# Kernel tuning notes

Hardware: AMD Instinct MI355X
Metric: run time of the kernel (lower is better)

## Reference

```python
import jax, jax.numpy as jnp
import numpy as np

TOPK = 9
NUM_CLASSES = 80
EPS = 1e-9
IMG = 1280
STRIDES = (8, 16, 32)


def _make_anchors():
    boxes = []
    for s in STRIDES:
        n = IMG // s
        c = (np.arange(n, dtype=np.float32) + 0.5) * s
        cy, cx = np.meshgrid(c, c, indexing='ij')
        cx = cx.reshape(-1); cy = cy.reshape(-1)
        half = s * 2.5
        boxes.append(np.stack([cx - half, cy - half, cx + half, cy + half], axis=-1))
    return jnp.asarray(np.concatenate(boxes, axis=0), jnp.float32)


def setup_inputs() -> dict:
    key = jax.random.key(0)
    k1, k2, k3 = jax.random.split(key, 3)
    B, M = 16, 64
    xy = jax.random.uniform(k1, (B, M, 2), jnp.float32, 0.0, 1100.0)
    wh = jax.random.uniform(k2, (B, M, 2), jnp.float32, 8.0, 180.0)
    gt_bboxes = jnp.concatenate([xy, xy + wh], axis=-1)
    gt_labels = jax.random.randint(k3, (B, M, 1), 0, NUM_CLASSES, jnp.int32)
    pad_gt_mask = (jnp.arange(M) < 56).astype(jnp.float32)[None, :, None] * jnp.ones((B, 1, 1), jnp.float32)
    return {
        'anchor_bboxes': _make_anchors(),
        'num_anchors_list': [25600, 6400, 1600],
        'gt_labels': gt_labels,
        'gt_bboxes': gt_bboxes,
        'pad_gt_mask': pad_gt_mask,
        'bg_index': NUM_CLASSES,
    }


def _atss(anchor_bboxes, num_anchors_list, gt_labels, gt_bboxes, pad_gt_mask, bg_index):
    B, M, _ = gt_bboxes.shape
    A = anchor_bboxes.shape[0]
    f32 = gt_bboxes.dtype

    # pairwise IoU [B, M, A]
    area_g = (gt_bboxes[..., 2] - gt_bboxes[..., 0]) * (gt_bboxes[..., 3] - gt_bboxes[..., 1])
    area_a = (anchor_bboxes[:, 2] - anchor_bboxes[:, 0]) * (anchor_bboxes[:, 3] - anchor_bboxes[:, 1])
    lt = jnp.maximum(gt_bboxes[..., None, :2], anchor_bboxes[None, None, :, :2])
    rb = jnp.minimum(gt_bboxes[..., None, 2:], anchor_bboxes[None, None, :, 2:])
    wh = jnp.clip(rb - lt, 0.0)
    overlap = wh[..., 0] * wh[..., 1]
    ious = overlap / (area_g[..., None] + area_a[None, None, :] - overlap + EPS)

    # center distances [B, M, A]
    gt_c = (gt_bboxes[..., :2] + gt_bboxes[..., 2:]) * 0.5
    an_c = (anchor_bboxes[:, :2] + anchor_bboxes[:, 2:]) * 0.5
    dist = jnp.linalg.norm(gt_c[:, :, None, :] - an_c[None, None, :, :], axis=-1)

    # per-pyramid-level topk (smallest distance)
    valid = pad_gt_mask > 0  # [B, M, 1]
    row = jnp.arange(B * M)[:, None]
    is_in_topk_parts, topk_idx_parts = [], []
    start = 0
    for n in num_anchors_list:
        d = dist[..., start:start + n]
        _, idxs = jax.lax.top_k(-d, TOPK)  # [B, M, TOPK]
        topk_idx_parts.append(idxs + start)
        idxs_m = jnp.where(valid, idxs, 0)
        counts = jnp.zeros((B * M, n), jnp.int32).at[row, idxs_m.reshape(B * M, TOPK)].add(1)
        counts = counts.reshape(B, M, n)
        is_in = jnp.where(counts > 1, 0, counts).astype(f32)  # zero duplicates (padded gts)
        is_in_topk_parts.append(is_in)
        start += n
    is_in_topk = jnp.concatenate(is_in_topk_parts, axis=-1)  # [B, M, A]
    topk_idxs = jnp.concatenate(topk_idx_parts, axis=-1)     # [B, M, TOPK * n_levels]

    # adaptive IoU threshold per gt: mean + std of candidate ious
    iou_candidates = ious * is_in_topk
    cand = jnp.take_along_axis(iou_candidates, topk_idxs, axis=-1)
    thr = cand.mean(axis=-1, keepdims=True) + jnp.std(cand, axis=-1, ddof=1, keepdims=True)
    is_in_topk = jnp.where(iou_candidates > thr, is_in_topk, jnp.zeros_like(is_in_topk))

    # anchor centers inside gt boxes [B, M, A]
    cx, cy = an_c[:, 0], an_c[:, 1]
    l = cx[None, None, :] - gt_bboxes[..., 0:1]
    t = cy[None, None, :] - gt_bboxes[..., 1:2]
    r = gt_bboxes[..., 2:3] - cx[None, None, :]
    b = gt_bboxes[..., 3:4] - cy[None, None, :]
    is_in_gts = (jnp.minimum(jnp.minimum(l, t), jnp.minimum(r, b)) > EPS).astype(f32)

    mask_positive = is_in_topk * is_in_gts * pad_gt_mask
    mps = mask_positive.sum(axis=-2)  # [B, A]

    # resolve anchors assigned to multiple gts via max-iou gt
    argm = ious.argmax(axis=-2)  # [B, A]
    is_max_iou = (jnp.arange(M)[None, :, None] == argm[:, None, :]).astype(f32)
    mask_multi = (mps[:, None, :] > 1)
    mask_positive = jnp.where(mask_multi, is_max_iou, mask_positive)
    mps = mask_positive.sum(axis=-2)

    assigned_gt_index = mask_positive.argmax(axis=-2)  # [B, A]
    assigned_labels = jnp.take_along_axis(gt_labels[..., 0], assigned_gt_index, axis=1)
    assigned_labels = jnp.where(mps > 0, assigned_labels, jnp.full_like(assigned_labels, bg_index))
    assigned_bboxes = jnp.take_along_axis(gt_bboxes, assigned_gt_index[..., None], axis=1)  # [B, A, 4]
    assigned_scores = jax.nn.one_hot(assigned_labels, NUM_CLASSES + 1, dtype=jnp.float32)[..., :NUM_CLASSES]
    return assigned_labels.astype(jnp.int32), assigned_bboxes, assigned_scores


def reference(anchor_bboxes, num_anchors_list, gt_labels, gt_bboxes, pad_gt_mask, bg_index):
    return _atss(anchor_bboxes, list(num_anchors_list), gt_labels, gt_bboxes, pad_gt_mask, bg_index)
```

## Files before the change

kernel.cpp:

```cpp
#include <hip/hip_runtime.h>
#include <stdint.h>


constexpr int A_TOT = 33600;
constexpr int NB    = 16;
constexpr int NM    = 64;
constexpr int NCLS  = 80;
constexpr int NBA   = NB * A_TOT;

__device__ __forceinline__ void anchor_geom(int a, float& cx, float& cy,
                                            float& half, float& area) {
    if (a < 25600) {
        int row = a / 160, col = a - row * 160;
        cx = (col + 0.5f) * 8.0f;  cy = (row + 0.5f) * 8.0f;
        half = 20.0f; area = 1600.0f;
    } else if (a < 32000) {
        int j = a - 25600; int row = j / 80, col = j - row * 80;
        cx = (col + 0.5f) * 16.0f; cy = (row + 0.5f) * 16.0f;
        half = 40.0f; area = 6400.0f;
    } else {
        int j = a - 32000; int row = j / 40, col = j - row * 40;
        cx = (col + 0.5f) * 32.0f; cy = (row + 0.5f) * 32.0f;
        half = 80.0f; area = 25600.0f;
    }
}

__device__ __forceinline__ float iou_box(float gx1, float gy1, float gx2, float gy2,
                                         float areag, float cx, float cy,
                                         float half, float areaa) {
    float ax1 = cx - half, ay1 = cy - half, ax2 = cx + half, ay2 = cy + half;
    float ltx = fmaxf(gx1, ax1), lty = fmaxf(gy1, ay1);
    float rbx = fminf(gx2, ax2), rby = fminf(gy2, ay2);
    float w = fmaxf(rbx - ltx, 0.0f), h = fmaxf(rby - lty, 0.0f);
    float ov = w * h;
    return ov / (areag + areaa - ov + 1e-9f);
}

template <int START, int N1, int S>
__device__ __forceinline__ void window_rank(int lane, float gcx, float gcy,
                                            uint64_t* keys36,
                                            uint64_t* cand_out ) {
    float tx = gcx / (float)S - 0.5f;
    float ty = gcy / (float)S - 0.5f;
    int c0 = (int)floorf(tx) - 2; c0 = min(max(c0, 0), N1 - 6);
    int r0 = (int)floorf(ty) - 2; r0 = min(max(r0, 0), N1 - 6);

    uint64_t mykey = ~0ull;
    if (lane < 36) {
        int wr = lane / 6, wc = lane - wr * 6;
        int row = r0 + wr, col = c0 + wc;
        float cx = (col + 0.5f) * (float)S;
        float cy = (row + 0.5f) * (float)S;
        float dx = gcx - cx, dy = gcy - cy;
        float d  = sqrtf(dx * dx + dy * dy);
        mykey = ((uint64_t)__float_as_uint(d) << 32)
              | (uint32_t)(START + row * N1 + col);
        keys36[lane] = mykey;
    }
    __syncthreads();

    if (lane < 36) {
        int rank = 0;
#pragma unroll
        for (int j = 0; j < 36; ++j)
            rank += (keys36[j] < mykey) ? 1 : 0;
        if (rank < 9) cand_out[rank] = mykey;
    }
    __syncthreads();
}

__global__ __launch_bounds__(64) void atss_topk(
    const float* __restrict__ gt_bboxes,
    const float* __restrict__ pad_mask,
    uint32_t* __restrict__ packed)
{
    int bm = blockIdx.x;
    if (pad_mask[bm] <= 0.0f) return;
    int b = bm >> 6, m = bm & 63;
    int lane = threadIdx.x;

    float4 g = ((const float4*)gt_bboxes)[bm];
    float gcx = (g.x + g.z) * 0.5f, gcy = (g.y + g.w) * 0.5f;
    float areag = (g.z - g.x) * (g.w - g.y);

    __shared__ uint64_t keys36[36];
    __shared__ uint64_t cand[27];
    __shared__ float    iou_s[27];
    __shared__ int      ok_s[27];

    window_rank<0,     160,  8>(lane, gcx, gcy, keys36, cand + 0);
    window_rank<25600,  80, 16>(lane, gcx, gcy, keys36, cand + 9);
    window_rank<32000,  40, 32>(lane, gcx, gcy, keys36, cand + 18);

    int aidx = 0; float iou = 0.0f;
    if (lane < 27) {
        aidx = (int)(cand[lane] & 0xffffffffu);
        float cx, cy, half, areaa;
        anchor_geom(aidx, cx, cy, half, areaa);
        iou = iou_box(g.x, g.y, g.z, g.w, areag, cx, cy, half, areaa);
        float l = cx - g.x, t = cy - g.y, r = g.z - cx, btm = g.w - cy;
        float mn = fminf(fminf(l, t), fminf(r, btm));
        iou_s[lane] = iou;
        ok_s[lane]  = (mn > 1e-9f) ? 1 : 0;
    }
    __syncthreads();

    float sum = 0.0f;
#pragma unroll
    for (int i = 0; i < 27; ++i) sum += iou_s[i];
    float mean = sum / 27.0f;
    float var = 0.0f;
#pragma unroll
    for (int i = 0; i < 27; ++i) { float d = iou_s[i] - mean; var += d * d; }
    float thr = mean + sqrtf(var / 26.0f);

    if (lane < 27 && ok_s[lane] && iou > thr) {
        atomicAdd(&packed[b * A_TOT + aidx], (1u << 20) | (uint32_t)m);
    }
}

__global__ __launch_bounds__(256) void atss_finalize(
    const float* __restrict__ gt_bboxes,
    const int*   __restrict__ gt_labels,
    const uint32_t* __restrict__ packed,
    float* __restrict__ out)
{
    int tid = blockIdx.x * 256 + threadIdx.x;
    int b = tid / A_TOT;
    int a = tid - b * A_TOT;

    uint32_t pk = packed[tid];
    int c = (int)(pk >> 20);
    int gidx = 0;
    if (c == 1) {
        gidx = (int)(pk & 0xfffffu);
    } else if (c > 1) {
        float cx, cy, half, areaa;
        anchor_geom(a, cx, cy, half, areaa);
        const float4* gb = (const float4*)(gt_bboxes) + b * NM;
        float best = -1.0f; int bi = 0;
        for (int mm = 0; mm < NM; ++mm) {
            float4 g = gb[mm];
            float areag = (g.z - g.x) * (g.w - g.y);
            float iou = iou_box(g.x, g.y, g.z, g.w, areag, cx, cy, half, areaa);
            if (iou > best) { best = iou; bi = mm; }
        }
        gidx = bi;
    }

    int label = (c > 0) ? gt_labels[b * NM + gidx] : NCLS;
    out[tid] = (float)label;
    float4 gsel = ((const float4*)gt_bboxes)[b * NM + gidx];
    ((float4*)(out + NBA))[tid] = gsel;

    __shared__ int lab_s[256];
    lab_s[threadIdx.x] = label;
    __syncthreads();

    float4* sc4 = (float4*)(out + (size_t)NBA * 5)
                + (size_t)blockIdx.x * (256 * 20);
#pragma unroll
    for (int i = 0; i < 20; ++i) {
        int k  = threadIdx.x + i * 256;
        int al = k / 20;
        int c4 = k - al * 20;
        int lab = lab_s[al];
        int base = c4 * 4;
        float4 v;
        v.x = (base + 0 == lab) ? 1.0f : 0.0f;
        v.y = (base + 1 == lab) ? 1.0f : 0.0f;
        v.z = (base + 2 == lab) ? 1.0f : 0.0f;
        v.w = (base + 3 == lab) ? 1.0f : 0.0f;
        sc4[k] = v;
    }
}

extern "C" void kernel_launch(void* const* d_in, const int* in_sizes, int n_in,
                              void* d_out, int out_size, void* d_ws, size_t ws_size,
                              hipStream_t stream) {
    const int*   gt_labels = (const int*)d_in[2];
    const float* gt_bboxes = (const float*)d_in[3];
    const float* pad_mask  = (const float*)d_in[4];
    float* out = (float*)d_out;

    uint32_t* packed = (uint32_t*)d_ws;

    hipMemsetAsync(packed, 0, (size_t)NBA * sizeof(uint32_t), stream);

    atss_topk<<<NB * NM, 64, 0, stream>>>(gt_bboxes, pad_mask, packed);

    atss_finalize<<<NBA / 256, 256, 0, stream>>>(
        gt_bboxes, gt_labels, packed, out);
}
```

Measured before the change: 198.5 us.

## Fuse topk and finalize kernels into one persistent kernel with grid barrier

Merges the per-gt top-k/threshold kernel and the per-anchor finalize kernel into a single persistent launch of 512 blocks. Two waves per block handle gt rows, then a software grid-wide barrier on an atomic counter separates the phases before blocks loop over the anchor tiles. This removes one kernel launch and its inter-kernel gap. In exchange it relies on all 512 blocks being co-resident for the spin barrier, which has a bounded-spin fallback, and gives each block a grid-stride loop with less parallelism in the output phase.

```diff
diff --git a/kernel.cpp b/kernel.cpp
--- a/kernel.cpp
+++ b/kernel.cpp
@@ -7,6 +7,8 @@
 constexpr int NM    = 64;
 constexpr int NCLS  = 80;
 constexpr int NBA   = NB * A_TOT;
+constexpr int GRID  = 512;
+constexpr int NTILE = NBA / 256;
 
 __device__ __forceinline__ void anchor_geom(int a, float& cx, float& cy,
                                             float& half, float& area) {
@@ -37,16 +39,16 @@
 }
 
 template <int START, int N1, int S>
-__device__ __forceinline__ void window_rank(int lane, float gcx, float gcy,
+__device__ __forceinline__ void window_rank(bool act, int lane,
+                                            float gcx, float gcy,
                                             uint64_t* keys36,
                                             uint64_t* cand_out ) {
-    float tx = gcx / (float)S - 0.5f;
-    float ty = gcy / (float)S - 0.5f;
-    int c0 = (int)floorf(tx) - 2; c0 = min(max(c0, 0), N1 - 6);
-    int r0 = (int)floorf(ty) - 2; r0 = min(max(r0, 0), N1 - 6);
-
     uint64_t mykey = ~0ull;
-    if (lane < 36) {
+    if (act && lane < 36) {
+        float tx = gcx / (float)S - 0.5f;
+        float ty = gcy / (float)S - 0.5f;
+        int c0 = (int)floorf(tx) - 2; c0 = min(max(c0, 0), N1 - 6);
+        int r0 = (int)floorf(ty) - 2; r0 = min(max(r0, 0), N1 - 6);
         int wr = lane / 6, wc = lane - wr * 6;
         int row = r0 + wr, col = c0 + wc;
         float cx = (col + 0.5f) * (float)S;
@@ -57,121 +59,137 @@
               | (uint32_t)(START + row * N1 + col);
         keys36[lane] = mykey;
     }
-    __syncthreads();
-
-    if (lane < 36) {
+    if (act && lane < 36) {
         int rank = 0;
 #pragma unroll
         for (int j = 0; j < 36; ++j)
             rank += (keys36[j] < mykey) ? 1 : 0;
         if (rank < 9) cand_out[rank] = mykey;
     }
-    __syncthreads();
-}
-
-__global__ __launch_bounds__(64) void atss_topk(
-    const float* __restrict__ gt_bboxes,
-    const float* __restrict__ pad_mask,
-    uint32_t* __restrict__ packed)
-{
-    int bm = blockIdx.x;
-    if (pad_mask[bm] <= 0.0f) return;
-    int b = bm >> 6, m = bm & 63;
-    int lane = threadIdx.x;
-
-    float4 g = ((const float4*)gt_bboxes)[bm];
-    float gcx = (g.x + g.z) * 0.5f, gcy = (g.y + g.w) * 0.5f;
-    float areag = (g.z - g.x) * (g.w - g.y);
-
-    __shared__ uint64_t keys36[36];
-    __shared__ uint64_t cand[27];
-    __shared__ float    iou_s[27];
-    __shared__ int      ok_s[27];
-
-    window_rank<0,     160,  8>(lane, gcx, gcy, keys36, cand + 0);
-    window_rank<25600,  80, 16>(lane, gcx, gcy, keys36, cand + 9);
-    window_rank<32000,  40, 32>(lane, gcx, gcy, keys36, cand + 18);
-
-    int aidx = 0; float iou = 0.0f;
-    if (lane < 27) {
-        aidx = (int)(cand[lane] & 0xffffffffu);
-        float cx, cy, half, areaa;
-        anchor_geom(aidx, cx, cy, half, areaa);
-        iou = iou_box(g.x, g.y, g.z, g.w, areag, cx, cy, half, areaa);
-        float l = cx - g.x, t = cy - g.y, r = g.z - cx, btm = g.w - cy;
-        float mn = fminf(fminf(l, t), fminf(r, btm));
-        iou_s[lane] = iou;
-        ok_s[lane]  = (mn > 1e-9f) ? 1 : 0;
-    }
-    __syncthreads();
-
-    float sum = 0.0f;
-#pragma unroll
-    for (int i = 0; i < 27; ++i) sum += iou_s[i];
-    float mean = sum / 27.0f;
-    float var = 0.0f;
-#pragma unroll
-    for (int i = 0; i < 27; ++i) { float d = iou_s[i] - mean; var += d * d; }
-    float thr = mean + sqrtf(var / 26.0f);
-
-    if (lane < 27 && ok_s[lane] && iou > thr) {
-        atomicAdd(&packed[b * A_TOT + aidx], (1u << 20) | (uint32_t)m);
-    }
-}
-
-__global__ __launch_bounds__(256) void atss_finalize(
+}
+
+__global__ __launch_bounds__(256, 4) void atss_fused(
     const float* __restrict__ gt_bboxes,
     const int*   __restrict__ gt_labels,
-    const uint32_t* __restrict__ packed,
+    const float* __restrict__ pad_mask,
+    uint32_t* __restrict__ packed,
+    uint32_t* __restrict__ barrier_ctr,
     float* __restrict__ out)
 {
-    int tid = blockIdx.x * 256 + threadIdx.x;
-    int b = tid / A_TOT;
-    int a = tid - b * A_TOT;
-
-    uint32_t pk = packed[tid];
-    int c = (int)(pk >> 20);
-    int gidx = 0;
-    if (c == 1) {
-        gidx = (int)(pk & 0xfffffu);
-    } else if (c > 1) {
-        float cx, cy, half, areaa;
-        anchor_geom(a, cx, cy, half, areaa);
-        const float4* gb = (const float4*)(gt_bboxes) + b * NM;
-        float best = -1.0f; int bi = 0;
-        for (int mm = 0; mm < NM; ++mm) {
-            float4 g = gb[mm];
-            float areag = (g.z - g.x) * (g.w - g.y);
-            float iou = iou_box(g.x, g.y, g.z, g.w, areag, cx, cy, half, areaa);
-            if (iou > best) { best = iou; bi = mm; }
-        }
-        gidx = bi;
-    }
-
-    int label = (c > 0) ? gt_labels[b * NM + gidx] : NCLS;
-    out[tid] = (float)label;
-    float4 gsel = ((const float4*)gt_bboxes)[b * NM + gidx];
-    ((float4*)(out + NBA))[tid] = gsel;
-
-    __shared__ int lab_s[256];
-    lab_s[threadIdx.x] = label;
+    const int tix  = threadIdx.x;
+    const int lane = tix & 63;
+    const int wave = tix >> 6;
+
+    __shared__ uint64_t keys36[2][36];
+    __shared__ uint64_t cand[2][27];
+    __shared__ float    iou_s[2][27];
+    __shared__ int      ok_s[2][27];
+    __shared__ int      lab_s[256];
+
+    if (wave < 2) {
+        int bm = blockIdx.x * 2 + wave;
+        int b = bm >> 6, m = bm & 63;
+        bool act = (pad_mask[bm] > 0.0f);
+
+        float4 g = ((const float4*)gt_bboxes)[bm];
+        float gcx = (g.x + g.z) * 0.5f, gcy = (g.y + g.w) * 0.5f;
+        float areag = (g.z - g.x) * (g.w - g.y);
+
+        window_rank<0,     160,  8>(act, lane, gcx, gcy, keys36[wave], cand[wave] + 0);
+        window_rank<25600,  80, 16>(act, lane, gcx, gcy, keys36[wave], cand[wave] + 9);
+        window_rank<32000,  40, 32>(act, lane, gcx, gcy, keys36[wave], cand[wave] + 18);
+
+        int aidx = 0; float iou = 0.0f;
+        if (act && lane < 27) {
+            aidx = (int)(cand[wave][lane] & 0xffffffffu);
+            float cx, cy, half, areaa;
+            anchor_geom(aidx, cx, cy, half, areaa);
+            iou = iou_box(g.x, g.y, g.z, g.w, areag, cx, cy, half, areaa);
+            float l = cx - g.x, t = cy - g.y, r = g.z - cx, btm = g.w - cy;
+            float mn = fminf(fminf(l, t), fminf(r, btm));
+            iou_s[wave][lane] = iou;
+            ok_s[wave][lane]  = (mn > 1e-9f) ? 1 : 0;
+        }
+        if (act) {
+            float sum = 0.0f;
+#pragma unroll
+            for (int i = 0; i < 27; ++i) sum += iou_s[wave][i];
+            float mean = sum / 27.0f;
+            float var = 0.0f;
+#pragma unroll
+            for (int i = 0; i < 27; ++i) { float d = iou_s[wave][i] - mean; var += d * d; }
+            float thr = mean + sqrtf(var / 26.0f);
+
+            if (lane < 27 && ok_s[wave][lane] && iou > thr) {
+                atomicAdd(&packed[b * A_TOT + aidx], (1u << 20) | (uint32_t)m);
+            }
+        }
+    }
+
     __syncthreads();
-
-    float4* sc4 = (float4*)(out + (size_t)NBA * 5)
-                + (size_t)blockIdx.x * (256 * 20);
-#pragma unroll
-    for (int i = 0; i < 20; ++i) {
-        int k  = threadIdx.x + i * 256;
-        int al = k / 20;
-        int c4 = k - al * 20;
-        int lab = lab_s[al];
-        int base = c4 * 4;
-        float4 v;
-        v.x = (base + 0 == lab) ? 1.0f : 0.0f;
-        v.y = (base + 1 == lab) ? 1.0f : 0.0f;
-        v.z = (base + 2 == lab) ? 1.0f : 0.0f;
-        v.w = (base + 3 == lab) ? 1.0f : 0.0f;
-        sc4[k] = v;
+    if (tix == 0) {
+        __threadfence();
+        atomicAdd(barrier_ctr, 1u);
+        int spins = 0;
+        uint32_t v;
+        do {
+            v = __hip_atomic_load(barrier_ctr, __ATOMIC_ACQUIRE,
+                                  __HIP_MEMORY_SCOPE_AGENT);
+        } while (v < (uint32_t)GRID && ++spins < 10000000);
+    }
+    __syncthreads();
+    __threadfence();
+
+    for (int tile = blockIdx.x; tile < NTILE; tile += GRID) {
+        int tid = tile * 256 + tix;
+        int b = tid / A_TOT;
+        int a = tid - b * A_TOT;
+
+        uint32_t pk = __hip_atomic_load(&packed[tid], __ATOMIC_RELAXED,
+                                        __HIP_MEMORY_SCOPE_AGENT);
+        int c = (int)(pk >> 20);
+        int gidx = 0;
+        if (c == 1) {
+            gidx = (int)(pk & 0xfffffu);
+        } else if (c > 1) {
+            float cx, cy, half, areaa;
+            anchor_geom(a, cx, cy, half, areaa);
+            const float4* gb = (const float4*)(gt_bboxes) + b * NM;
+            float best = -1.0f; int bi = 0;
+            for (int mm = 0; mm < NM; ++mm) {
+                float4 g = gb[mm];
+                float areag = (g.z - g.x) * (g.w - g.y);
+                float iou = iou_box(g.x, g.y, g.z, g.w, areag, cx, cy, half, areaa);
+                if (iou > best) { best = iou; bi = mm; }
+            }
+            gidx = bi;
+        }
+
+        int label = (c > 0) ? gt_labels[b * NM + gidx] : NCLS;
+        out[tid] = (float)label;
+        float4 gsel = ((const float4*)gt_bboxes)[b * NM + gidx];
+        ((float4*)(out + NBA))[tid] = gsel;
+
+        lab_s[tix] = label;
+        __syncthreads();
+
+        float4* sc4 = (float4*)(out + (size_t)NBA * 5)
+                    + (size_t)tile * (256 * 20);
+#pragma unroll
+        for (int i = 0; i < 20; ++i) {
+            int k  = tix + i * 256;
+            int al = k / 20;
+            int c4 = k - al * 20;
+            int lab = lab_s[al];
+            int base = c4 * 4;
+            float4 v;
+            v.x = (base + 0 == lab) ? 1.0f : 0.0f;
+            v.y = (base + 1 == lab) ? 1.0f : 0.0f;
+            v.z = (base + 2 == lab) ? 1.0f : 0.0f;
+            v.w = (base + 3 == lab) ? 1.0f : 0.0f;
+            sc4[k] = v;
+        }
+        __syncthreads();
     }
 }
 
@@ -181,14 +199,13 @@
     const int*   gt_labels = (const int*)d_in[2];
     const float* gt_bboxes = (const float*)d_in[3];
     const float* pad_mask  = (const float*)d_in[4];
-    float* out = (float*)d_out;
+    float*       out       = (float*)d_out;
 
     uint32_t* packed = (uint32_t*)d_ws;
-
-    hipMemsetAsync(packed, 0, (size_t)NBA * sizeof(uint32_t), stream);
-
-    atss_topk<<<NB * NM, 64, 0, stream>>>(gt_bboxes, pad_mask, packed);
-
-    atss_finalize<<<NBA / 256, 256, 0, stream>>>(
-        gt_bboxes, gt_labels, packed, out);
-}
+    uint32_t* ctr    = (uint32_t*)((char*)d_ws + (size_t)NBA * sizeof(uint32_t));
+
+    hipMemsetAsync(d_ws, 0, (size_t)NBA * sizeof(uint32_t) + 64, stream);
+
+    atss_fused<<<GRID, 256, 0, stream>>>(
+        gt_bboxes, gt_labels, pad_mask, packed, ctr, out);
+}
```

Result: slower. 256.5 us (+29.2%).
